# Performance work log

Hardware: AMD Instinct MI355X
Metric: run time of the kernel (lower is better)

Reference implementation:

```python
import jax, jax.numpy as jnp
import numpy as np
import math

DIFF = True   # params['diff'] -> kind='random_walk'
SHIFT = 0.0   # params['shift']
MIN_WINDOW = 10
EPS = 1e-6


def _window_sizes(T):
    ws = []
    cur = math.log10(MIN_WINDOW)
    end = math.log10(T - 1)
    while cur < end:
        w = int(10 ** cur)
        if MIN_WINDOW <= w <= T - 1:
            ws.append(w)
        cur += 0.25
    if T not in ws:
        ws.append(T)
    return sorted(set(ws))


def _hurst_random_walk(x):
    B, T = x.shape
    ws = _window_sizes(T)  # static python list (shapes are static)
    rs_list = []
    for w in ws:
        n = T // w
        seg = x[:, : n * w].reshape(B, n, w)            # (B, n, w)
        d = seg[..., 1:] - seg[..., :-1]                # (B, n, w-1)
        mean_inc = (seg[..., -1] - seg[..., 0]) / (w - 1)
        dev = d - mean_inc[..., None]
        Z = jnp.cumsum(dev, axis=-1)                    # rescaled-range scan
        R = jnp.max(Z, axis=-1) - jnp.min(Z, axis=-1)   # (B, n)
        S = jnp.std(d, axis=-1, ddof=1)                 # unbiased std
        rs_list.append(jnp.mean(R / (S + EPS), axis=-1))
    RS = jnp.stack(rs_list, axis=1)                     # (B, K)
    X = jnp.log10(jnp.asarray(ws, dtype=x.dtype) + EPS) # (K,)
    Y = jnp.log10(RS + EPS)
    Xc = X - jnp.mean(X)
    denom = jnp.sum(Xc * Xc)
    H = jnp.sum((Y - jnp.mean(Y, axis=1, keepdims=True)) * Xc, axis=1) / (denom + EPS)
    H = jnp.where(jnp.isfinite(H), H, jnp.asarray(1.0, x.dtype))
    return H


def setup_inputs() -> dict:
    key = jax.random.key(0)
    x = jax.random.normal(key, (8192, 4096), dtype=jnp.float32)
    return {"x": x}


def reference(x):
    H = _hurst_random_walk(x)
    return (H + SHIFT)[:, None]  # (B, 1)
```

## Files before the change

kernel.cpp:

```cpp
#include <hip/hip_runtime.h>
#include <math.h>
#include <utility>

#define TLEN 4096
#define NW   12
#define BLOCK 256
#define EPSF 1e-6f

typedef float v2f __attribute__((ext_vector_type(2)));

__device__ const float XC_TAB[NW] = {
    -1.3608041f, -1.1303552f, -0.8694424f, -0.6126161f,
    -0.3608041f, -0.1128308f,  0.1388830f,  0.3889322f,
     0.6391959f,  0.8891277f,  1.1391578f,  1.2515558f };
__device__ const float INVN_TAB[NW] = {
    1.0f/409.0f, 1.0f/240.0f, 1.0f/132.0f, 1.0f/73.0f,
    1.0f/40.0f,  1.0f/23.0f,  1.0f/12.0f,  1.0f/7.0f,
    0.25f, 0.5f, 1.0f, 1.0f };
#define INV_DEN 0.11577579f
#define LOG10_2 0.30102999566f

__device__ __forceinline__ float max3f(float a, float b, float c) {
    float r; asm("v_max3_f32 %0, %1, %2, %3" : "=v"(r) : "v"(a), "v"(b), "v"(c)); return r;
}
__device__ __forceinline__ float min3f(float a, float b, float c) {
    float r; asm("v_min3_f32 %0, %1, %2, %3" : "=v"(r) : "v"(a), "v"(b), "v"(c)); return r;
}
__device__ __forceinline__ v2f pk_fma(v2f a, v2f b, v2f c) {
    v2f d; asm("v_pk_fma_f32 %0, %1, %2, %3" : "=v"(d) : "v"(a), "v"(b), "v"(c)); return d;
}
__device__ __forceinline__ v2f pk_add(v2f a, v2f b) {
    v2f d; asm("v_pk_add_f32 %0, %1, %2" : "=v"(d) : "v"(a), "v"(b)); return d;
}

__device__ __forceinline__ float wave_reduce_sum(float v) {
    #pragma unroll
    for (int o = 32; o > 0; o >>= 1) v += __shfl_xor(v, o, 64);
    return v;
}
template<int G>
__device__ __forceinline__ float reduce_leaders(float v) {
    #pragma unroll
    for (int o = G; o < 64; o <<= 1) v += __shfl_xor(v, o, 64);
    return v;
}

template<bool FIX_LO, bool FIX_HI>
__device__ __forceinline__ float seg_rs2(const float* __restrict__ row,
                                         const float* __restrict__ P2,
                                         int b, int W, float m, float invwm2,
                                         float mx, float mn) {
    float plo = P2[b >> 1];
    if constexpr (FIX_LO) { float d = row[b] - row[b - 1]; plo = fmaf(d, d, plo); }
    float phi = P2[(b + W - 1) >> 1];
    if constexpr (FIX_HI) { float d = row[b + W - 1] - row[b + W - 2]; phi = fmaf(d, d, phi); }
    float ss  = phi - plo;
    float var = fmaf(-(float)(W - 1) * m, m, ss) * invwm2;
    float S   = __builtin_amdgcn_sqrtf(fmaxf(var, 0.0f));
    return (mx - mn) * __builtin_amdgcn_rcpf(S + EPSF);
}

template<int LO, int HI, int JB>
__device__ __forceinline__ void chunk_fold(const float4 q, float nm, float& mx, float& mn) {
    if constexpr (LO <= HI) {
        constexpr int NV = HI - LO + 1;
        float v[NV];
        #pragma unroll
        for (int r = 0; r < NV; ++r)
            v[r] = fmaf((float)(JB + LO + r), nm, (&q.x)[LO + r]);
        if constexpr (NV == 1) { mx = fmaxf(mx, v[0]); mn = fminf(mn, v[0]); }
        else if constexpr (NV == 2) { mx = max3f(mx, v[0], v[1]); mn = min3f(mn, v[0], v[1]); }
        else if constexpr (NV == 3) { mx = fmaxf(mx, max3f(v[0], v[1], v[2]));
                                      mn = fminf(mn, min3f(v[0], v[1], v[2])); }
        else { mx = max3f(max3f(mx, v[0], v[1]), v[2], v[3]);
               mn = min3f(min3f(mn, v[0], v[1]), v[2], v[3]); }
    }
}

__device__ __forceinline__ float w10_task(const float* __restrict__ row,
                                          const float* __restrict__ P2,
                                          int t, bool pair) {
    const int b = t * 20;
    const int h = b >> 1;
    const float4* p = (const float4*)(row + b);
    float4 q0 = p[0], q1 = p[1], q2 = p[2];
    float acc;
    {
        const float m = (q2.y - q0.x) * (1.0f / 9.0f), nm = -m;
        float v1 = fmaf(1.0f, nm, q0.y);
        float v2 = fmaf(2.0f, nm, q0.z);
        float v3 = fmaf(3.0f, nm, q0.w);
        float mx = max3f(v1, v2, v3), mn = min3f(v1, v2, v3);
        float v4 = fmaf(4.0f, nm, q1.x);
        float v5 = fmaf(5.0f, nm, q1.y);
        float v6 = fmaf(6.0f, nm, q1.z);
        float v7 = fmaf(7.0f, nm, q1.w);
        mx = max3f(mx, v4, v5); mn = min3f(mn, v4, v5);
        mx = max3f(mx, v6, v7); mn = min3f(mn, v6, v7);
        float v8 = fmaf(8.0f, nm, q2.x);
        float v9 = fmaf(9.0f, nm, q2.y);
        mx = max3f(mx, v8, v9); mn = min3f(mn, v8, v9);
        float d9 = q2.y - q2.x;
        float ss = fmaf(d9, d9, P2[h + 4]) - P2[h];
        float var = fmaf(-9.0f * m, m, ss) * 0.125f;
        float S = __builtin_amdgcn_sqrtf(fmaxf(var, 0.0f));
        acc = (mx - mn) * __builtin_amdgcn_rcpf(S + EPSF);
    }
    if (pair) {
        float4 q3 = p[3], q4 = p[4];
        const float m = (q4.w - q2.z) * (1.0f / 9.0f), nm = -m;
        float v1 = fmaf(1.0f, nm, q2.w);
        float v2 = fmaf(2.0f, nm, q3.x);
        float v3 = fmaf(3.0f, nm, q3.y);
        float mx = max3f(v1, v2, v3), mn = min3f(v1, v2, v3);
        float v4 = fmaf(4.0f, nm, q3.z);
        float v5 = fmaf(5.0f, nm, q3.w);
        float v6 = fmaf(6.0f, nm, q4.x);
        float v7 = fmaf(7.0f, nm, q4.y);
        mx = max3f(mx, v4, v5); mn = min3f(mn, v4, v5);
        mx = max3f(mx, v6, v7); mn = min3f(mn, v6, v7);
        float v8 = fmaf(8.0f, nm, q4.z);
        float v9 = fmaf(9.0f, nm, q4.w);
        mx = max3f(mx, v8, v9); mn = min3f(mn, v8, v9);
        float d9 = q4.w - q4.z;
        float ss = fmaf(d9, d9, P2[h + 9]) - P2[h + 5];
        float var = fmaf(-9.0f * m, m, ss) * 0.125f;
        float S = __builtin_amdgcn_sqrtf(fmaxf(var, 0.0f));
        acc += (mx - mn) * __builtin_amdgcn_rcpf(S + EPSF);
    }
    return acc;
}

template<int W, int NSEG, int C>
__device__ __forceinline__ void mchunk_step(const float4* __restrict__ p,
                                            const float (&nm)[NSEG],
                                            float (&mx)[NSEG], float (&mn)[NSEG]) {
    constexpr int E0 = 4 * C;
    constexpr int K0 = E0 / W;
    constexpr int SA = K0 * W;
    constexpr int LOA = (SA == E0) ? 1 : 0;
    constexpr int HIA_ = SA + W - 1 - E0;
    constexpr int HIA = HIA_ < 3 ? HIA_ : 3;
    float4 q = p[C];
    if constexpr (K0 < NSEG)
        chunk_fold<LOA, HIA, E0 - SA>(q, nm[K0], mx[K0], mn[K0]);
    constexpr bool HASB = (K0 + 1 < NSEG) && (SA + W + 1 - E0 <= 3);
    if constexpr (HASB) {
        constexpr int SB = SA + W;
        chunk_fold<SB + 1 - E0, 3, E0 - SB>(q, nm[K0 + 1], mx[K0 + 1], mn[K0 + 1]);
    }
}

template<int W, int NSEG, int... Cs>
__device__ __forceinline__ void mseg_all(const float4* __restrict__ p,
                                         const float (&nm)[NSEG],
                                         float (&mx)[NSEG], float (&mn)[NSEG],
                                         std::integer_sequence<int, Cs...>) {
    (mchunk_step<W, NSEG, Cs>(p, nm, mx, mn), ...);
}

template<int W, int NSEG>
__device__ __forceinline__ float mseg_task_odd(const float* __restrict__ row,
                                               const float* __restrict__ P2, int b) {
    constexpr int NCH = (W * NSEG + 3) / 4;
    constexpr float invwm2 = 1.0f / (float)(W - 2);
    const float4* p = (const float4*)(row + b);
    float nm[NSEG], m[NSEG], mx[NSEG], mn[NSEG];
    #pragma unroll
    for (int k = 0; k < NSEG; ++k) {
        float a0 = row[b + k * W];
        float a1 = row[b + k * W + W - 1];
        m[k] = (a1 - a0) * (1.0f / (float)(W - 1));
        nm[k] = -m[k];
        mx[k] = -INFINITY; mn[k] = INFINITY;
    }
    mseg_all<W, NSEG>(p, nm, mx, mn, std::make_integer_sequence<int, NCH>{});
    float acc = 0.0f;
    #pragma unroll
    for (int k = 0; k < NSEG; ++k) {
        float r = (k & 1)
            ? seg_rs2<true,  true >(row, P2, b + k * W, W, m[k], invwm2, mx[k], mn[k])
            : seg_rs2<false, false>(row, P2, b + k * W, W, m[k], invwm2, mx[k], mn[k]);
        acc += r;
    }
    return acc;
}

template<int W, int A, int G>
__device__ __forceinline__ void seg_strided_pk(const float* __restrict__ row, int b, int lane,
                                               float nm, float& mx, float& mn) {
    constexpr int NCH  = (A + W - 1) / 4 + 1;
    constexpr int HIL  = (A + W - 1) & 3;
    constexpr int MAIN_END = (HIL == 3) ? NCH : NCH - 1;
    constexpr int NFULL = MAIN_END - 1;
    constexpr int FULL  = NFULL / G;
    constexpr int REM   = NFULL % G;
    const float4* p = (const float4*)(row + (b - A));
    mx = -INFINITY; mn = INFINITY;
    const float4* pl = p + (1 + lane);
    v2f jc; jc.x = (float)(4 * (1 + lane) - A); jc.y = jc.x + 1.0f;
    const v2f nm2   = {nm, nm};
    const v2f nm2x2 = {nm + nm, nm + nm};
    const v2f step  = {(float)(4 * G), (float)(4 * G)};
    #pragma unroll
    for (int i = 0; i < FULL; ++i) {
        float4 q = pl[i * G];
        v2f q01 = {q.x, q.y}, q23 = {q.z, q.w};
        v2f t01 = pk_fma(jc, nm2, q01);
        v2f t23 = pk_fma(jc, nm2, pk_add(q23, nm2x2));
        mx = max3f(max3f(mx, t01.x, t01.y), t23.x, t23.y);
        mn = min3f(min3f(mn, t01.x, t01.y), t23.x, t23.y);
        jc = pk_add(jc, step);
    }
    if constexpr (REM > 0) {
        if (lane < REM) {
            float4 q = pl[FULL * G];
            v2f q01 = {q.x, q.y}, q23 = {q.z, q.w};
            v2f t01 = pk_fma(jc, nm2, q01);
            v2f t23 = pk_fma(jc, nm2, pk_add(q23, nm2x2));
            mx = max3f(max3f(mx, t01.x, t01.y), t23.x, t23.y);
            mn = min3f(min3f(mn, t01.x, t01.y), t23.x, t23.y);
        }
    }
    if constexpr (A < 3) {
        if (lane == 0) chunk_fold<A + 1, 3, -A>(p[0], nm, mx, mn);
    }
    if constexpr (HIL != 3) {
        if (lane == 1) chunk_fold<0, HIL, 4 * (NCH - 1) - A>(p[NCH - 1], nm, mx, mn);
    }
}

template<int W, int A, int G>
__device__ __forceinline__ float group_seg(const float* __restrict__ row,
                                           const float* __restrict__ P2,
                                           int s, int lane) {
    const int b = s * W;
    float a0 = row[b], a1 = row[b + W - 1];
    float m = (a1 - a0) * (1.0f / (float)(W - 1));
    float nm = -m;
    float mx, mn;
    seg_strided_pk<W, A, G>(row, b, lane, nm, mx, mn);
    #pragma unroll
    for (int o = G / 2; o > 0; o >>= 1) {
        mx = fmaxf(mx, __shfl_xor(mx, o, G));
        mn = fminf(mn, __shfl_xor(mn, o, G));
    }
    float r = seg_rs2<(A & 1) != 0, ((A + W - 1) & 1) != 0>(
        row, P2, b, W, m, 1.0f / (float)(W - 2), mx, mn);
    return (lane == 0) ? r : 0.0f;
}

__global__ __launch_bounds__(BLOCK) void hurst_kernel(const float* __restrict__ x,
                                                      float* __restrict__ out) {
    __shared__ __align__(16) float row[TLEN];
    __shared__ __align__(16) float P2[TLEN / 2];
    __shared__ float rs_sum[NW];
    __shared__ float wred[8];

    const int tid = threadIdx.x;
    const int r = blockIdx.x;
    const int w = tid >> 6, l = tid & 63;

    const float4* src = (const float4*)(x + (size_t)r * TLEN);
    float4* dst = (float4*)row;
    #pragma unroll
    for (int i = 0; i < TLEN / 4 / BLOCK; ++i)
        dst[tid + i * BLOCK] = src[tid + i * BLOCK];
    if (tid < NW) rs_sum[tid] = 0.0f;
    __syncthreads();

    {
        const int base = tid * 16;
        float v[17];
        const float4* rp = (const float4*)(row + base);
        float4 q0 = rp[0], q1 = rp[1], q2 = rp[2], q3 = rp[3];
        v[0]=q0.x;  v[1]=q0.y;  v[2]=q0.z;  v[3]=q0.w;
        v[4]=q1.x;  v[5]=q1.y;  v[6]=q1.z;  v[7]=q1.w;
        v[8]=q2.x;  v[9]=q2.y;  v[10]=q2.z; v[11]=q2.w;
        v[12]=q3.x; v[13]=q3.y; v[14]=q3.z; v[15]=q3.w;
        v[16] = row[(base + 16 < TLEN) ? base + 16 : TLEN - 1];

        float pl[8];
        float c = 0.0f;
        #pragma unroll
        for (int j = 0; j < 16; ++j) {
            if ((j & 1) == 0) pl[j >> 1] = c;
            float d = v[j + 1] - v[j];
            c = fmaf(d, d, c);
        }
        const float total = c;
        float incl = total;
        #pragma unroll
        for (int o = 1; o < 64; o <<= 1) {
            float u = __shfl_up(incl, o, 64);
            if (l >= o) incl += u;
        }
        if (l == 63) wred[w] = incl;
        __syncthreads();
        float off = incl - total;
        #pragma unroll
        for (int w2 = 0; w2 < 4; ++w2)
            if (w2 < w) off += wred[w2];
        float4* pp = (float4*)(P2 + tid * 8);
        pp[0] = make_float4(off + pl[0], off + pl[1], off + pl[2], off + pl[3]);
        pp[1] = make_float4(off + pl[4], off + pl[5], off + pl[6], off + pl[7]);
    }
    __syncthreads();


    {
        float a = 0.0f;
        if (tid < 204)       a = w10_task(row, P2, tid, true);
        else if (tid == 204) a = w10_task(row, P2, 204, false);
        a = wave_reduce_sum(a);
        if (l == 0) atomicAdd(&rs_sum[0], a);
    }
    if (w == 0) {
        float a = (l < 60) ? mseg_task_odd<17, 4>(row, P2, l * 68) : 0.0f;
        a = wave_reduce_sum(a);
        if (l == 0) atomicAdd(&rs_sum[1], a);
    } else if (w == 1) {
        float a = (l < 33) ? mseg_task_odd<31, 4>(row, P2, l * 124) : 0.0f;
        a = wave_reduce_sum(a);
        if (l == 0) atomicAdd(&rs_sum[2], a);
    }
    {
        const int g = tid >> 2, gl = tid & 3;
        float a = group_seg<56, 0, 4>(row, P2, g, gl);
        if (g + 64 < 73) a += group_seg<56, 0, 4>(row, P2, g + 64, gl);
        a = reduce_leaders<4>(a);
        if (l == 0) atomicAdd(&rs_sum[3], a);
    }
    {
        const int g = tid >> 3, gl = tid & 7;
        float a = group_seg<100, 0, 8>(row, P2, g, gl);
        if (g + 32 < 40) a += group_seg<100, 0, 8>(row, P2, g + 32, gl);
        a = reduce_leaders<8>(a);
        if (l == 0) atomicAdd(&rs_sum[4], a);
    }
    {
        const int g4 = (tid >> 4) & 3, gl16 = tid & 15;
        float a = 0.0f;
        if (w == 0) {
            a = group_seg<177, 0, 16>(row, P2, 4 * g4, gl16);
            if (g4 < 2) a += group_seg<177, 0, 16>(row, P2, 4 * (g4 + 4), gl16);
        } else if (w == 1) {
            a = group_seg<177, 1, 16>(row, P2, 4 * g4 + 1, gl16);
            if (g4 < 2) a += group_seg<177, 1, 16>(row, P2, 4 * (g4 + 4) + 1, gl16);
        } else if (w == 2) {
            a = group_seg<177, 2, 16>(row, P2, 4 * g4 + 2, gl16);
            if (g4 < 2) a += group_seg<177, 2, 16>(row, P2, 4 * (g4 + 4) + 2, gl16);
        } else {
            a = group_seg<177, 3, 16>(row, P2, 4 * g4 + 3, gl16);
            if (g4 < 1) a += group_seg<177, 3, 16>(row, P2, 4 * (g4 + 4) + 3, gl16);
        }
        a = reduce_leaders<16>(a);
        if (l == 0) atomicAdd(&rs_sum[5], a);
    }
    if (tid < 192) {
        float a = group_seg<316, 0, 16>(row, P2, tid >> 4, tid & 15);
        a = reduce_leaders<16>(a);
        if (l == 0) atomicAdd(&rs_sum[6], a);
    }
    {
        const int gh = (tid >> 5) & 1, gl32 = tid & 31;
        float a = 0.0f;
        if (w == 0)      a = group_seg<562, 0, 32>(row, P2, 0 + 2 * gh, gl32);
        else if (w == 1) a = group_seg<562, 0, 32>(row, P2, 4 + 2 * gh, gl32);
        else if (w == 2) a = group_seg<562, 2, 32>(row, P2, 1 + 2 * gh, gl32);
        else if (gh == 0) a = group_seg<562, 2, 32>(row, P2, 5, gl32);
        a = reduce_leaders<32>(a);
        if (l == 0) atomicAdd(&rs_sum[7], a);
    }
    if (tid < 128) {
        float a = group_seg<1000, 0, 32>(row, P2, tid >> 5, tid & 31);
        a = reduce_leaders<32>(a);
        if (l == 0) atomicAdd(&rs_sum[8], a);
    }


    {
        const int half = tid >> 7, hl = tid & 127;
        const int b = half ? 1778 : 0;
        float m = (row[b + 1777] - row[b]) * (1.0f / 1777.0f);
        float nm = -m, mx, mn;
        if (half == 0) seg_strided_pk<1778, 0, 128>(row, 0,    hl, nm, mx, mn);
        else           seg_strided_pk<1778, 2, 128>(row, 1778, hl, nm, mx, mn);
        #pragma unroll
        for (int o = 32; o > 0; o >>= 1) {
            mx = fmaxf(mx, __shfl_xor(mx, o, 64));
            mn = fminf(mn, __shfl_xor(mn, o, 64));
        }
        if (l == 0) { wred[w * 2] = mx; wred[w * 2 + 1] = mn; }
        __syncthreads();
        if ((tid & 127) == 0) {
            const int wb = tid >> 6;
            float MX = fmaxf(wred[wb * 2],     wred[wb * 2 + 2]);
            float MN = fminf(wred[wb * 2 + 1], wred[wb * 2 + 3]);
            atomicAdd(&rs_sum[9],
                      seg_rs2<false, true>(row, P2, b, 1778, m, 1.0f / 1776.0f, MX, MN));
        }
        __syncthreads();
    }
    {
        float m = (row[3161] - row[0]) * (1.0f / 3161.0f);
        float nm = -m, mx, mn;
        seg_strided_pk<3162, 0, 256>(row, 0, tid, nm, mx, mn);
        #pragma unroll
        for (int o = 32; o > 0; o >>= 1) {
            mx = fmaxf(mx, __shfl_xor(mx, o, 64));
            mn = fminf(mn, __shfl_xor(mn, o, 64));
        }
        if (l == 0) { wred[w * 2] = mx; wred[w * 2 + 1] = mn; }
        __syncthreads();
        if (tid == 0) {
            float MX = fmaxf(fmaxf(wred[0], wred[2]), fmaxf(wred[4], wred[6]));
            float MN = fminf(fminf(wred[1], wred[3]), fminf(wred[5], wred[7]));
            atomicAdd(&rs_sum[10],
                      seg_rs2<false, true>(row, P2, 0, 3162, m, 1.0f / 3160.0f, MX, MN));
        }
        __syncthreads();
    }
    {
        float m = (row[4095] - row[0]) * (1.0f / 4095.0f);
        float nm = -m, mx, mn;
        seg_strided_pk<4096, 0, 256>(row, 0, tid, nm, mx, mn);
        #pragma unroll
        for (int o = 32; o > 0; o >>= 1) {
            mx = fmaxf(mx, __shfl_xor(mx, o, 64));
            mn = fminf(mn, __shfl_xor(mn, o, 64));
        }
        if (l == 0) { wred[w * 2] = mx; wred[w * 2 + 1] = mn; }
        __syncthreads();
        if (tid == 0) {
            float MX = fmaxf(fmaxf(wred[0], wred[2]), fmaxf(wred[4], wred[6]));
            float MN = fminf(fminf(wred[1], wred[3]), fminf(wred[5], wred[7]));
            atomicAdd(&rs_sum[11],
                      seg_rs2<false, true>(row, P2, 0, 4096, m, 1.0f / 4094.0f, MX, MN));
        }
        __syncthreads();
    }

    if (tid < 64) {
        float t = 0.0f;
        if (tid < NW) {
            float rs = fmaf(rs_sum[tid], INVN_TAB[tid], EPSF);
            t = __builtin_amdgcn_logf(rs) * (LOG10_2) * XC_TAB[tid];
        }
        t = wave_reduce_sum(t);
        if (tid == 0) {
            float h = t * INV_DEN;
            if (!isfinite(h)) h = 1.0f;
            out[r] = h;
        }
    }
}

extern "C" void kernel_launch(void* const* d_in, const int* in_sizes, int n_in,
                              void* d_out, int out_size, void* d_ws, size_t ws_size,
                              hipStream_t stream) {
    const float* x = (const float*)d_in[0];
    float* out = (float*)d_out;
    const int B = out_size;
    hipLaunchKernelGGL(hurst_kernel, dim3(B), dim3(BLOCK), 0, stream, x, out);
}
```

Baseline: 93.07 us.

## Shrink prefix-sum table to stride-4 and rebalance waves for higher occupancy

Stores the sum-of-squared-differences prefix only every fourth element, which shrinks the shared-memory table by half, and recovers the skipped terms with up to three extra differences per segment boundary. It also adds a launch-bounds occupancy hint of 7, hoists the strided float4 loads ahead of the arithmetic, and reassigns several window groups to different waves to balance the work. The aim is to fit more blocks per CU and hide LDS latency. The cost is extra boundary arithmetic per segment and possible register pressure from the hoisted loads under the tighter launch bound.

Measured after the change: 90.05 us. 3.2% less time.

```diff
diff --git a/kernel.cpp b/kernel.cpp
--- a/kernel.cpp
+++ b/kernel.cpp
@@ -45,15 +45,30 @@
     return v;
 }
 
-template<bool FIX_LO, bool FIX_HI>
+template<int FLO, int FHI>
 __device__ __forceinline__ float seg_rs2(const float* __restrict__ row,
-                                         const float* __restrict__ P2,
+                                         const float* __restrict__ P4,
                                          int b, int W, float m, float invwm2,
                                          float mx, float mn) {
-    float plo = P2[b >> 1];
-    if constexpr (FIX_LO) { float d = row[b] - row[b - 1]; plo = fmaf(d, d, plo); }
-    float phi = P2[(b + W - 1) >> 1];
-    if constexpr (FIX_HI) { float d = row[b + W - 1] - row[b + W - 2]; phi = fmaf(d, d, phi); }
+    float plo = P4[b >> 2];
+    if constexpr (FLO > 0) {
+        const int k0 = b - FLO;
+        #pragma unroll
+        for (int t = 0; t < FLO; ++t) {
+            float d = row[k0 + t + 1] - row[k0 + t];
+            plo = fmaf(d, d, plo);
+        }
+    }
+    const int e = b + W - 1;
+    float phi = P4[e >> 2];
+    if constexpr (FHI > 0) {
+        const int k0 = e - FHI;
+        #pragma unroll
+        for (int t = 0; t < FHI; ++t) {
+            float d = row[k0 + t + 1] - row[k0 + t];
+            phi = fmaf(d, d, phi);
+        }
+    }
     float ss  = phi - plo;
     float var = fmaf(-(float)(W - 1) * m, m, ss) * invwm2;
     float S   = __builtin_amdgcn_sqrtf(fmaxf(var, 0.0f));
@@ -78,10 +93,10 @@
 }
 
 __device__ __forceinline__ float w10_task(const float* __restrict__ row,
-                                          const float* __restrict__ P2,
+                                          const float* __restrict__ P4,
                                           int t, bool pair) {
     const int b = t * 20;
-    const int h = b >> 1;
+    const int h = t * 5;
     const float4* p = (const float4*)(row + b);
     float4 q0 = p[0], q1 = p[1], q2 = p[2];
     float acc;
@@ -100,8 +115,8 @@
         float v8 = fmaf(8.0f, nm, q2.x);
         float v9 = fmaf(9.0f, nm, q2.y);
         mx = max3f(mx, v8, v9); mn = min3f(mn, v8, v9);
-        float d9 = q2.y - q2.x;
-        float ss = fmaf(d9, d9, P2[h + 4]) - P2[h];
+        float d8 = q2.y - q2.x;
+        float ss = fmaf(d8, d8, P4[h + 2]) - P4[h];
         float var = fmaf(-9.0f * m, m, ss) * 0.125f;
         float S = __builtin_amdgcn_sqrtf(fmaxf(var, 0.0f));
         acc = (mx - mn) * __builtin_amdgcn_rcpf(S + EPSF);
@@ -122,8 +137,14 @@
         float v8 = fmaf(8.0f, nm, q4.z);
         float v9 = fmaf(9.0f, nm, q4.w);
         mx = max3f(mx, v8, v9); mn = min3f(mn, v8, v9);
-        float d9 = q4.w - q4.z;
-        float ss = fmaf(d9, d9, P2[h + 9]) - P2[h + 5];
+        float d8  = q2.y - q2.x;
+        float d9  = q2.z - q2.y;
+        float d16 = q4.y - q4.x;
+        float d17 = q4.z - q4.y;
+        float d18 = q4.w - q4.z;
+        float plo = fmaf(d9, d9, fmaf(d8, d8, P4[h + 2]));
+        float phi = fmaf(d18, d18, fmaf(d17, d17, fmaf(d16, d16, P4[h + 4])));
+        float ss = phi - plo;
         float var = fmaf(-9.0f * m, m, ss) * 0.125f;
         float S = __builtin_amdgcn_sqrtf(fmaxf(var, 0.0f));
         acc += (mx - mn) * __builtin_amdgcn_rcpf(S + EPSF);
@@ -159,11 +180,23 @@
     (mchunk_step<W, NSEG, Cs>(p, nm, mx, mn), ...);
 }
 
+template<int W, int NSEG, int... Ks>
+__device__ __forceinline__ float mseg_rs_all(const float* __restrict__ row,
+                                             const float* __restrict__ P4, int b,
+                                             const float (&m)[NSEG],
+                                             const float (&mx)[NSEG], const float (&mn)[NSEG],
+                                             std::integer_sequence<int, Ks...>) {
+    constexpr float invwm2 = 1.0f / (float)(W - 2);
+    float acc = 0.0f;
+    ((acc += seg_rs2<(W * Ks) & 3, (W * Ks + W - 1) & 3>(
+          row, P4, b + Ks * W, W, m[Ks], invwm2, mx[Ks], mn[Ks])), ...);
+    return acc;
+}
+
 template<int W, int NSEG>
 __device__ __forceinline__ float mseg_task_odd(const float* __restrict__ row,
-                                               const float* __restrict__ P2, int b) {
+                                               const float* __restrict__ P4, int b) {
     constexpr int NCH = (W * NSEG + 3) / 4;
-    constexpr float invwm2 = 1.0f / (float)(W - 2);
     const float4* p = (const float4*)(row + b);
     float nm[NSEG], m[NSEG], mx[NSEG], mn[NSEG];
     #pragma unroll
@@ -175,15 +208,8 @@
         mx[k] = -INFINITY; mn[k] = INFINITY;
     }
     mseg_all<W, NSEG>(p, nm, mx, mn, std::make_integer_sequence<int, NCH>{});
-    float acc = 0.0f;
-    #pragma unroll
-    for (int k = 0; k < NSEG; ++k) {
-        float r = (k & 1)
-            ? seg_rs2<true,  true >(row, P2, b + k * W, W, m[k], invwm2, mx[k], mn[k])
-            : seg_rs2<false, false>(row, P2, b + k * W, W, m[k], invwm2, mx[k], mn[k]);
-        acc += r;
-    }
-    return acc;
+    return mseg_rs_all<W, NSEG>(row, P4, b, m, mx, mn,
+                                std::make_integer_sequence<int, NSEG>{});
 }
 
 template<int W, int A, int G>
@@ -195,16 +221,21 @@
     constexpr int NFULL = MAIN_END - 1;
     constexpr int FULL  = NFULL / G;
     constexpr int REM   = NFULL % G;
-    const float4* p = (const float4*)(row + (b - A));
+    constexpr int NB    = FULL + (REM > 0 ? 1 : 0);
+    const float4* p  = (const float4*)(row + (b - A));
+    const float4* pl = p + (1 + lane);
+    float4 qs[NB > 0 ? NB : 1];
+    #pragma unroll
+    for (int i = 0; i < FULL; ++i) qs[i] = pl[i * G];
+    if constexpr (REM > 0) { if (lane < REM) qs[FULL] = pl[FULL * G]; }
     mx = -INFINITY; mn = INFINITY;
-    const float4* pl = p + (1 + lane);
     v2f jc; jc.x = (float)(4 * (1 + lane) - A); jc.y = jc.x + 1.0f;
     const v2f nm2   = {nm, nm};
     const v2f nm2x2 = {nm + nm, nm + nm};
     const v2f step  = {(float)(4 * G), (float)(4 * G)};
     #pragma unroll
     for (int i = 0; i < FULL; ++i) {
-        float4 q = pl[i * G];
+        float4 q = qs[i];
         v2f q01 = {q.x, q.y}, q23 = {q.z, q.w};
         v2f t01 = pk_fma(jc, nm2, q01);
         v2f t23 = pk_fma(jc, nm2, pk_add(q23, nm2x2));
@@ -214,7 +245,7 @@
     }
     if constexpr (REM > 0) {
         if (lane < REM) {
-            float4 q = pl[FULL * G];
+            float4 q = qs[FULL];
             v2f q01 = {q.x, q.y}, q23 = {q.z, q.w};
             v2f t01 = pk_fma(jc, nm2, q01);
             v2f t23 = pk_fma(jc, nm2, pk_add(q23, nm2x2));
@@ -232,7 +263,7 @@
 
 template<int W, int A, int G>
 __device__ __forceinline__ float group_seg(const float* __restrict__ row,
-                                           const float* __restrict__ P2,
+                                           const float* __restrict__ P4,
                                            int s, int lane) {
     const int b = s * W;
     float a0 = row[b], a1 = row[b + W - 1];
@@ -245,15 +276,15 @@
         mx = fmaxf(mx, __shfl_xor(mx, o, G));
         mn = fminf(mn, __shfl_xor(mn, o, G));
     }
-    float r = seg_rs2<(A & 1) != 0, ((A + W - 1) & 1) != 0>(
-        row, P2, b, W, m, 1.0f / (float)(W - 2), mx, mn);
+    float r = seg_rs2<A, (A + W - 1) & 3>(
+        row, P4, b, W, m, 1.0f / (float)(W - 2), mx, mn);
     return (lane == 0) ? r : 0.0f;
 }
 
-__global__ __launch_bounds__(BLOCK) void hurst_kernel(const float* __restrict__ x,
-                                                      float* __restrict__ out) {
+__global__ __launch_bounds__(BLOCK, 7) void hurst_kernel(const float* __restrict__ x,
+                                                         float* __restrict__ out) {
     __shared__ __align__(16) float row[TLEN];
-    __shared__ __align__(16) float P2[TLEN / 2];
+    __shared__ __align__(16) float P4[TLEN / 4];
     __shared__ float rs_sum[NW];
     __shared__ float wred[8];
 
@@ -280,11 +311,11 @@
         v[12]=q3.x; v[13]=q3.y; v[14]=q3.z; v[15]=q3.w;
         v[16] = row[(base + 16 < TLEN) ? base + 16 : TLEN - 1];
 
-        float pl[8];
+        float pl4[4];
         float c = 0.0f;
         #pragma unroll
         for (int j = 0; j < 16; ++j) {
-            if ((j & 1) == 0) pl[j >> 1] = c;
+            if ((j & 3) == 0) pl4[j >> 2] = c;
             float d = v[j + 1] - v[j];
             c = fmaf(d, d, c);
         }
@@ -301,40 +332,43 @@
         #pragma unroll
         for (int w2 = 0; w2 < 4; ++w2)
             if (w2 < w) off += wred[w2];
-        float4* pp = (float4*)(P2 + tid * 8);
-        pp[0] = make_float4(off + pl[0], off + pl[1], off + pl[2], off + pl[3]);
-        pp[1] = make_float4(off + pl[4], off + pl[5], off + pl[6], off + pl[7]);
+        float4* pp = (float4*)(P4 + tid * 4);
+        pp[0] = make_float4(off + pl4[0], off + pl4[1], off + pl4[2], off + pl4[3]);
     }
     __syncthreads();
 
 
     {
         float a = 0.0f;
-        if (tid < 204)       a = w10_task(row, P2, tid, true);
-        else if (tid == 204) a = w10_task(row, P2, 204, false);
+        if (tid < 204)       a = w10_task(row, P4, tid, true);
+        else if (tid == 204) a = w10_task(row, P4, 204, false);
         a = wave_reduce_sum(a);
         if (l == 0) atomicAdd(&rs_sum[0], a);
     }
     if (w == 0) {
-        float a = (l < 60) ? mseg_task_odd<17, 4>(row, P2, l * 68) : 0.0f;
+        float a = (l < 60) ? mseg_task_odd<17, 4>(row, P4, l * 68) : 0.0f;
         a = wave_reduce_sum(a);
         if (l == 0) atomicAdd(&rs_sum[1], a);
     } else if (w == 1) {
-        float a = (l < 33) ? mseg_task_odd<31, 4>(row, P2, l * 124) : 0.0f;
+        float a = (l < 33) ? mseg_task_odd<31, 4>(row, P4, l * 124) : 0.0f;
         a = wave_reduce_sum(a);
         if (l == 0) atomicAdd(&rs_sum[2], a);
     }
     {
         const int g = tid >> 2, gl = tid & 3;
-        float a = group_seg<56, 0, 4>(row, P2, g, gl);
-        if (g + 64 < 73) a += group_seg<56, 0, 4>(row, P2, g + 64, gl);
+        float a = group_seg<56, 0, 4>(row, P4, g, gl);
+        if (w == 2) {
+            int s2 = 64 + ((tid - 128) >> 2);
+            if (s2 < 73) a += group_seg<56, 0, 4>(row, P4, s2, gl);
+        }
         a = reduce_leaders<4>(a);
         if (l == 0) atomicAdd(&rs_sum[3], a);
     }
     {
         const int g = tid >> 3, gl = tid & 7;
-        float a = group_seg<100, 0, 8>(row, P2, g, gl);
-        if (g + 32 < 40) a += group_seg<100, 0, 8>(row, P2, g + 32, gl);
+        float a = group_seg<100, 0, 8>(row, P4, g, gl);
+        if (w == 3)
+            a += group_seg<100, 0, 8>(row, P4, 32 + ((tid - 192) >> 3), gl);
         a = reduce_leaders<8>(a);
         if (l == 0) atomicAdd(&rs_sum[4], a);
     }
@@ -342,38 +376,46 @@
         const int g4 = (tid >> 4) & 3, gl16 = tid & 15;
         float a = 0.0f;
         if (w == 0) {
-            a = group_seg<177, 0, 16>(row, P2, 4 * g4, gl16);
-            if (g4 < 2) a += group_seg<177, 0, 16>(row, P2, 4 * (g4 + 4), gl16);
+            a = group_seg<177, 0, 16>(row, P4, 4 * g4, gl16);
+            if (g4 < 2) a += group_seg<177, 0, 16>(row, P4, 4 * (g4 + 4), gl16);
         } else if (w == 1) {
-            a = group_seg<177, 1, 16>(row, P2, 4 * g4 + 1, gl16);
-            if (g4 < 2) a += group_seg<177, 1, 16>(row, P2, 4 * (g4 + 4) + 1, gl16);
+            a = group_seg<177, 1, 16>(row, P4, 4 * g4 + 1, gl16);
+            if (g4 < 2) a += group_seg<177, 1, 16>(row, P4, 4 * (g4 + 4) + 1, gl16);
         } else if (w == 2) {
-            a = group_seg<177, 2, 16>(row, P2, 4 * g4 + 2, gl16);
-            if (g4 < 2) a += group_seg<177, 2, 16>(row, P2, 4 * (g4 + 4) + 2, gl16);
+            a = group_seg<177, 2, 16>(row, P4, 4 * g4 + 2, gl16);
+            if (g4 < 2) a += group_seg<177, 2, 16>(row, P4, 4 * (g4 + 4) + 2, gl16);
         } else {
-            a = group_seg<177, 3, 16>(row, P2, 4 * g4 + 3, gl16);
-            if (g4 < 1) a += group_seg<177, 3, 16>(row, P2, 4 * (g4 + 4) + 3, gl16);
+            a = group_seg<177, 3, 16>(row, P4, 4 * g4 + 3, gl16);
+            if (g4 < 1) a += group_seg<177, 3, 16>(row, P4, 4 * (g4 + 4) + 3, gl16);
         }
         a = reduce_leaders<16>(a);
         if (l == 0) atomicAdd(&rs_sum[5], a);
     }
-    if (tid < 192) {
-        float a = group_seg<316, 0, 16>(row, P2, tid >> 4, tid & 15);
+    if (w != 1) {
+        const int g4 = (tid >> 4) & 3, gl16 = tid & 15;
+        const int base = (w == 0) ? 0 : (w == 2) ? 4 : 8;
+        float a = group_seg<316, 0, 16>(row, P4, base + g4, gl16);
         a = reduce_leaders<16>(a);
         if (l == 0) atomicAdd(&rs_sum[6], a);
     }
     {
         const int gh = (tid >> 5) & 1, gl32 = tid & 31;
-        float a = 0.0f;
-        if (w == 0)      a = group_seg<562, 0, 32>(row, P2, 0 + 2 * gh, gl32);
-        else if (w == 1) a = group_seg<562, 0, 32>(row, P2, 4 + 2 * gh, gl32);
-        else if (w == 2) a = group_seg<562, 2, 32>(row, P2, 1 + 2 * gh, gl32);
-        else if (gh == 0) a = group_seg<562, 2, 32>(row, P2, 5, gl32);
-        a = reduce_leaders<32>(a);
-        if (l == 0) atomicAdd(&rs_sum[7], a);
-    }
-    if (tid < 128) {
-        float a = group_seg<1000, 0, 32>(row, P2, tid >> 5, tid & 31);
+        if (w == 2) {
+            float a = group_seg<562, 0, 32>(row, P4, 2 * gh, gl32);
+            a += group_seg<562, 0, 32>(row, P4, 4 + 2 * gh, gl32);
+            a = reduce_leaders<32>(a);
+            if (l == 0) atomicAdd(&rs_sum[7], a);
+        } else if (w == 3) {
+            float a = group_seg<562, 2, 32>(row, P4, 1 + 2 * gh, gl32);
+            if (gh == 0) a += group_seg<562, 2, 32>(row, P4, 5, gl32);
+            a = reduce_leaders<32>(a);
+            if (l == 0) atomicAdd(&rs_sum[7], a);
+        }
+    }
+    if (w >= 2) {
+        const int gh = (tid >> 5) & 1, gl32 = tid & 31;
+        const int s = (w == 2 ? 0 : 2) + gh;
+        float a = group_seg<1000, 0, 32>(row, P4, s, gl32);
         a = reduce_leaders<32>(a);
         if (l == 0) atomicAdd(&rs_sum[8], a);
     }
@@ -397,8 +439,10 @@
             const int wb = tid >> 6;
             float MX = fmaxf(wred[wb * 2],     wred[wb * 2 + 2]);
             float MN = fminf(wred[wb * 2 + 1], wred[wb * 2 + 3]);
-            atomicAdd(&rs_sum[9],
-                      seg_rs2<false, true>(row, P2, b, 1778, m, 1.0f / 1776.0f, MX, MN));
+            float v;
+            if (tid == 0) v = seg_rs2<0, 1>(row, P4, 0,    1778, m, 1.0f / 1776.0f, MX, MN);
+            else          v = seg_rs2<2, 3>(row, P4, 1778, 1778, m, 1.0f / 1776.0f, MX, MN);
+            atomicAdd(&rs_sum[9], v);
         }
         __syncthreads();
     }
@@ -417,7 +461,7 @@
             float MX = fmaxf(fmaxf(wred[0], wred[2]), fmaxf(wred[4], wred[6]));
             float MN = fminf(fminf(wred[1], wred[3]), fminf(wred[5], wred[7]));
             atomicAdd(&rs_sum[10],
-                      seg_rs2<false, true>(row, P2, 0, 3162, m, 1.0f / 3160.0f, MX, MN));
+                      seg_rs2<0, 1>(row, P4, 0, 3162, m, 1.0f / 3160.0f, MX, MN));
         }
         __syncthreads();
     }
@@ -436,7 +480,7 @@
             float MX = fmaxf(fmaxf(wred[0], wred[2]), fmaxf(wred[4], wred[6]));
             float MN = fminf(fminf(wred[1], wred[3]), fminf(wred[5], wred[7]));
             atomicAdd(&rs_sum[11],
-                      seg_rs2<false, true>(row, P2, 0, 4096, m, 1.0f / 4094.0f, MX, MN));
+                      seg_rs2<0, 3>(row, P4, 0, 4096, m, 1.0f / 4094.0f, MX, MN));
         }
         __syncthreads();
     }
```
